# Kernel tuning notes

Hardware: AMD Instinct MI355X
Metric: run time of the kernel (lower is better)

## Reference

```python
import jax, jax.numpy as jnp
import numpy as np

B = 2
D_MODEL = 256
D_FFN = 1024
N_LEVELS = 4
N_HEADS = 8
N_POINTS = 4
D_HEAD = D_MODEL // N_HEADS
SHAPES = np.array([[128, 128], [64, 64], [32, 32], [16, 16]], dtype=np.int32)  # (H, W) per level
LEN = int(SHAPES.prod(axis=1).sum())  # 21760
EPS = 1e-5


def _layer_norm(x, g, b):
    m = jnp.mean(x, axis=-1, keepdims=True)
    v = jnp.mean(jnp.square(x - m), axis=-1, keepdims=True)
    return (x - m) * jax.lax.rsqrt(v + EPS) * g + b


def _bilinear_gather(v_l, loc, H, W):
    # v_l: [B, H*W, NH, DH]; loc: [B, L, NH, NP, 2] in normalized [0,1] coords (x, y)
    # grid_sample(align_corners=False, padding_mode=zeros) semantics: pixel = loc * size - 0.5
    x = loc[..., 0] * W - 0.5
    y = loc[..., 1] * H - 0.5
    x0 = jnp.floor(x)
    y0 = jnp.floor(y)
    dx = x - x0
    dy = y - y0
    x0i = x0.astype(jnp.int32)
    y0i = y0.astype(jnp.int32)
    b_ix = jnp.arange(v_l.shape[0])[:, None, None, None]
    h_ix = jnp.arange(v_l.shape[2])[None, None, :, None]

    def corner(xi, yi, w):
        valid = (xi >= 0) & (xi < W) & (yi >= 0) & (yi < H)
        idx = jnp.clip(yi, 0, H - 1) * W + jnp.clip(xi, 0, W - 1)
        v = v_l[b_ix, idx, h_ix]  # [B, L, NH, NP, DH]
        return v * (w * valid.astype(v.dtype))[..., None]

    return (corner(x0i, y0i, (1 - dx) * (1 - dy))
            + corner(x0i + 1, y0i, dx * (1 - dy))
            + corner(x0i, y0i + 1, (1 - dx) * dy)
            + corner(x0i + 1, y0i + 1, dx * dy))


def _forward(src, pos, reference_points,
             w_off, b_off, w_attn, b_attn, w_val, b_val, w_out, b_out,
             ln1_g, ln1_b, w1, b1, w2, b2, ln2_g, ln2_b,
             spatial_shapes, level_start_index, padding_mask):
    shapes = np.asarray(spatial_shapes)        # static per-level (H, W)
    starts = np.asarray(level_start_index)     # static level offsets
    Bsz, L, _ = src.shape

    # ---- MSDeformAttn ----
    q = src + pos                              # with_pos_embed
    value = src @ w_val + b_val
    value = jnp.where(padding_mask[..., None], 0.0, value)
    value = value.reshape(Bsz, L, N_HEADS, D_HEAD)

    off = (q @ w_off + b_off).reshape(Bsz, L, N_HEADS, N_LEVELS, N_POINTS, 2)
    attn = (q @ w_attn + b_attn).reshape(Bsz, L, N_HEADS, N_LEVELS * N_POINTS)
    attn = jax.nn.softmax(attn, axis=-1).reshape(Bsz, L, N_HEADS, N_LEVELS, N_POINTS)

    wh = jnp.asarray(shapes[:, ::-1].copy(), dtype=src.dtype)  # [NL, 2] = (W, H)
    loc = reference_points[:, :, None, :, None, :] + off / wh[None, None, None, :, None, :]

    out = jnp.zeros((Bsz, L, N_HEADS, D_HEAD), src.dtype)
    for l in range(N_LEVELS):
        H, W = int(shapes[l, 0]), int(shapes[l, 1])
        s = int(starts[l])
        v_l = value[:, s:s + H * W]                          # [B, H*W, NH, DH]
        sampled = _bilinear_gather(v_l, loc[:, :, :, l], H, W)  # [B, L, NH, NP, DH]
        out = out + (sampled * attn[:, :, :, l][..., None]).sum(axis=3)
    attn_out = out.reshape(Bsz, L, D_MODEL) @ w_out + b_out

    # ---- residual + LN + FFN + residual + LN (dropout = identity in eval) ----
    x = _layer_norm(src + attn_out, ln1_g, ln1_b)
    ffn = jax.nn.relu(x @ w1 + b1) @ w2 + b2
    return _layer_norm(x + ffn, ln2_g, ln2_b)


def setup_inputs() -> dict:
    key = jax.random.key(0)
    ks = jax.random.split(key, 16)
    s = 0.02
    n_off = N_HEADS * N_LEVELS * N_POINTS
    level_start = np.concatenate([[0], SHAPES.prod(axis=1).cumsum()[:-1]]).astype(np.int32)
    return {
        "src": jax.random.normal(ks[0], (B, LEN, D_MODEL), jnp.float32),
        "pos": jax.random.normal(ks[1], (B, LEN, D_MODEL), jnp.float32),
        "reference_points": jax.random.uniform(ks[2], (B, LEN, N_LEVELS, 2), jnp.float32),
        "spatial_shapes": jnp.asarray(SHAPES),
        "level_start_index": jnp.asarray(level_start),
        "padding_mask": jnp.zeros((B, LEN), jnp.bool_),
        "w_off": jax.random.normal(ks[3], (D_MODEL, n_off * 2), jnp.float32) * s,
        "b_off": jax.random.normal(ks[4], (n_off * 2,), jnp.float32) * 0.5,
        "w_attn": jax.random.normal(ks[5], (D_MODEL, n_off), jnp.float32) * s,
        "b_attn": jnp.zeros((n_off,), jnp.float32),
        "w_val": jax.random.normal(ks[6], (D_MODEL, D_MODEL), jnp.float32) * s,
        "b_val": jnp.zeros((D_MODEL,), jnp.float32),
        "w_out": jax.random.normal(ks[7], (D_MODEL, D_MODEL), jnp.float32) * s,
        "b_out": jnp.zeros((D_MODEL,), jnp.float32),
        "ln1_g": jnp.ones((D_MODEL,), jnp.float32),
        "ln1_b": jnp.zeros((D_MODEL,), jnp.float32),
        "w1": jax.random.normal(ks[8], (D_MODEL, D_FFN), jnp.float32) * s,
        "b1": jnp.zeros((D_FFN,), jnp.float32),
        "w2": jax.random.normal(ks[9], (D_FFN, D_MODEL), jnp.float32) * s,
        "b2": jnp.zeros((D_MODEL,), jnp.float32),
        "ln2_g": jnp.ones((D_MODEL,), jnp.float32),
        "ln2_b": jnp.zeros((D_MODEL,), jnp.float32),
    }


def reference(src, pos, reference_points, spatial_shapes, level_start_index, padding_mask,
              w_off, b_off, w_attn, b_attn, w_val, b_val, w_out, b_out,
              ln1_g, ln1_b, w1, b1, w2, b2, ln2_g, ln2_b):
    return _forward(src, pos, reference_points,
                    w_off, b_off, w_attn, b_attn, w_val, b_val, w_out, b_out,
                    ln1_g, ln1_b, w1, b1, w2, b2, ln2_g, ln2_b,
                    spatial_shapes, level_start_index, padding_mask)
```

## Files before the change

kernel.cpp:

```cpp
#include <hip/hip_runtime.h>
#include <hip/hip_bf16.h>

#define BSZ      2
#define LTOK     21760
#define NTOK     (BSZ * LTOK)
#define DMODEL   256
#define DFFN     1024

typedef __attribute__((ext_vector_type(8))) short short8;
typedef __attribute__((ext_vector_type(4))) float f32x4;

__device__ __forceinline__ unsigned short f2bf(float x) {
    __hip_bfloat16 h = __float2bfloat16(x);
    return *reinterpret_cast<unsigned short*>(&h);
}
__device__ __forceinline__ float bf2f(unsigned short u) {
    union { unsigned int i; float f; } c; c.i = ((unsigned int)u) << 16; return c.f;
}
__device__ __forceinline__ float bflo(unsigned int u) {
    union { unsigned int i; float f; } c; c.i = u << 16; return c.f;
}
__device__ __forceinline__ float bfhi(unsigned int u) {
    union { unsigned int i; float f; } c; c.i = u & 0xffff0000u; return c.f;
}

__device__ __forceinline__ void gload_lds16(const void* g, void* l) {
    __builtin_amdgcn_global_load_lds(
        (const __attribute__((address_space(1))) unsigned int*)g,
        (__attribute__((address_space(3))) unsigned int*)l, 16, 0, 0);
}

#define TM 128
#define TN 256
#define TBK 32
#define BUFSZ (TM * TBK + TN * TBK)
#define EBS 264

__device__ __forceinline__ void stage_tile(
    const unsigned short* aR0, const unsigned short* aR1,
    const unsigned short* bR0, const unsigned short* bR1,
    const unsigned short* bR2, const unsigned short* bR3,
    int k0, unsigned short* sA, unsigned short* sB, int sr)
{
    gload_lds16(aR0 + k0, &sA[(sr + 0)  * 512]);
    gload_lds16(aR1 + k0, &sA[(sr + 4)  * 512]);
    gload_lds16(bR0 + k0, &sB[(sr + 0)  * 512]);
    gload_lds16(bR1 + k0, &sB[(sr + 4)  * 512]);
    gload_lds16(bR2 + k0, &sB[(sr + 8)  * 512]);
    gload_lds16(bR3 + k0, &sB[(sr + 12) * 512]);
}

__device__ __forceinline__ void compute_tile(
    const unsigned short* sA, const unsigned short* sB,
    int lane, int wm, int wn, f32x4 acc[4][8])
{
    short8 af[4], bfr[8];
    #pragma unroll
    for (int i = 0; i < 4; ++i)
        af[i] = *(const short8*)&sA[(wm * 4 + i) * 512 + lane * 8];
    #pragma unroll
    for (int j = 0; j < 8; ++j)
        bfr[j] = *(const short8*)&sB[(wn * 8 + j) * 512 + lane * 8];
    #pragma unroll
    for (int i = 0; i < 4; ++i)
        #pragma unroll
        for (int j = 0; j < 8; ++j)
            acc[i][j] = __builtin_amdgcn_mfma_f32_16x16x32_bf16(
                af[i], bfr[j], acc[i][j], 0, 0, 0);
}

__device__ __forceinline__ void gemm_core(
    const unsigned short* __restrict__ A,
    const unsigned short* __restrict__ Bt,
    unsigned short* smem,
    int bm, int bn, int N, int K,
    int tid, int lane, int wm, int wn,
    f32x4 acc[4][8])
{
    const int sr = tid >> 6;
    const int fr = lane & 15;
    const int fk = (lane >> 4) * 8;

    const unsigned short* aR0 = A + (size_t)(bm + (sr + 0) * 16 + fr) * K + fk;
    const unsigned short* aR1 = A + (size_t)(bm + (sr + 4) * 16 + fr) * K + fk;
    const unsigned short* bR0 = Bt + (size_t)min(bn + (sr + 0)  * 16 + fr, N - 1) * K + fk;
    const unsigned short* bR1 = Bt + (size_t)min(bn + (sr + 4)  * 16 + fr, N - 1) * K + fk;
    const unsigned short* bR2 = Bt + (size_t)min(bn + (sr + 8)  * 16 + fr, N - 1) * K + fk;
    const unsigned short* bR3 = Bt + (size_t)min(bn + (sr + 12) * 16 + fr, N - 1) * K + fk;

    unsigned short* sA0 = smem;
    unsigned short* sB0 = smem + TM * TBK;
    unsigned short* sA1 = smem + BUFSZ;
    unsigned short* sB1 = smem + BUFSZ + TM * TBK;

    stage_tile(aR0, aR1, bR0, bR1, bR2, bR3, 0, sA0, sB0, sr);
    __syncthreads();

    for (int k0 = 0; k0 < K; k0 += 2 * TBK) {
        if (k0 + TBK < K)
            stage_tile(aR0, aR1, bR0, bR1, bR2, bR3, k0 + TBK, sA1, sB1, sr);
        compute_tile(sA0, sB0, lane, wm, wn, acc);
        __syncthreads();
        if (k0 + 2 * TBK < K)
            stage_tile(aR0, aR1, bR0, bR1, bR2, bR3, k0 + 2 * TBK, sA0, sB0, sr);
        compute_tile(sA1, sB1, lane, wm, wn, acc);
        __syncthreads();
    }
}

__global__ __launch_bounds__(256, 2) void gemm_mfma(
    const unsigned short* __restrict__ A,
    const unsigned short* __restrict__ Bt, const float* __restrict__ bias,
    unsigned short* __restrict__ Cb,
    int M, int N, int K, int relu)
{
    __shared__ __align__(16) unsigned short smem[2 * BUFSZ];
    const int tid  = threadIdx.x;
    const int lane = tid & 63;
    const int wave = tid >> 6;
    const int wm = wave >> 1, wn = wave & 1;
    const int bm = blockIdx.y * TM;
    const int bn = blockIdx.x * TN;

    f32x4 acc[4][8];
    #pragma unroll
    for (int i = 0; i < 4; ++i)
        #pragma unroll
        for (int j = 0; j < 8; ++j)
            acc[i][j] = (f32x4){0.f, 0.f, 0.f, 0.f};

    gemm_core(A, Bt, smem, bm, bn, N, K, tid, lane, wm, wn, acc);

    const int r0 = (lane >> 4) * 4;
    const int c0 = lane & 15;
    unsigned short* eb = smem;
    #pragma unroll
    for (int i = 0; i < 4; ++i) {
        if (i) __syncthreads();
        #pragma unroll
        for (int j = 0; j < 8; ++j) {
            const int col = bn + wn * 128 + j * 16 + c0;
            const float bj = (col < N) ? bias[col] : 0.f;
            #pragma unroll
            for (int r = 0; r < 4; ++r) {
                float v = acc[i][j][r] + bj;
                if (relu) v = fmaxf(v, 0.f);
                eb[(wm * 16 + r0 + r) * EBS + wn * 128 + j * 16 + c0] = f2bf(v);
            }
        }
        __syncthreads();
        #pragma unroll
        for (int qq = 0; qq < 4; ++qq) {
            const int q  = tid + qq * 256;
            const int rl = q >> 5;
            const int ch = q & 31;
            const int grow = bm + (rl >> 4) * 64 + i * 16 + (rl & 15);
            const int colb = bn + ch * 8;
            if (colb < N)
                *(uint4*)&Cb[(size_t)grow * N + colb] =
                    *(const uint4*)&eb[rl * EBS + ch * 8];
        }
    }
}

__global__ __launch_bounds__(256, 2) void gemm_proj(
    const unsigned short* __restrict__ A0, const unsigned short* __restrict__ B0,
    const float* __restrict__ bias0, unsigned short* __restrict__ C0,
    const unsigned char* __restrict__ mask,
    const unsigned short* __restrict__ A1, const unsigned short* __restrict__ B1,
    const float* __restrict__ bias1, unsigned short* __restrict__ C1)
{
    __shared__ __align__(16) unsigned short smem[2 * BUFSZ];
    const int tid  = threadIdx.x;
    const int lane = tid & 63;
    const int wave = tid >> 6;
    const int wm = wave >> 1, wn = wave & 1;
    const int bm = blockIdx.y * TM;
    const int bx = blockIdx.x;

    const int isv = (bx == 0);
    const unsigned short* A    = isv ? A0 : A1;
    const unsigned short* Bt   = isv ? B0 : B1;
    const float*          bias = isv ? bias0 : bias1;
    const int N  = isv ? 256 : 384;
    const int bn = isv ? 0 : (bx - 1) * 256;
    const int K  = 256;

    f32x4 acc[4][8];
    #pragma unroll
    for (int i = 0; i < 4; ++i)
        #pragma unroll
        for (int j = 0; j < 8; ++j)
            acc[i][j] = (f32x4){0.f, 0.f, 0.f, 0.f};

    gemm_core(A, Bt, smem, bm, bn, N, K, tid, lane, wm, wn, acc);

    const int r0 = (lane >> 4) * 4;
    const int c0 = lane & 15;
    unsigned short* eb = smem;
    #pragma unroll
    for (int i = 0; i < 4; ++i) {
        if (i) __syncthreads();
        #pragma unroll
        for (int j = 0; j < 8; ++j) {
            const int col = bn + wn * 128 + j * 16 + c0;
            const float bj = (col < N) ? bias[col] : 0.f;
            #pragma unroll
            for (int r = 0; r < 4; ++r) {
                const int row = bm + wm * 64 + i * 16 + r0 + r;
                float v = acc[i][j][r] + bj;
                if (isv && mask[row]) v = 0.f;
                eb[(wm * 16 + r0 + r) * EBS + wn * 128 + j * 16 + c0] = f2bf(v);
            }
        }
        __syncthreads();
        #pragma unroll
        for (int qq = 0; qq < 4; ++qq) {
            const int q  = tid + qq * 256;
            const int rl = q >> 5;
            const int ch = q & 31;
            const int grow = bm + (rl >> 4) * 64 + i * 16 + (rl & 15);
            const int colb = bn + ch * 8;
            if (colb < N) {
                const uint4 val = *(const uint4*)&eb[rl * EBS + ch * 8];
                if (isv) {
                    const int bb   = grow >= LTOK;
                    const int srow = grow - bb * LTOK;
                    const int hcol = ch >> 2;
                    const int d    = (ch & 3) * 8;
                    *(uint4*)&C0[((size_t)(bb * 8 + hcol) * LTOK + srow) * 32 + d] = val;
                } else {
                    *(uint4*)&C1[(size_t)grow * 384 + colb] = val;
                }
            }
        }
    }
}

__global__ __launch_bounds__(256, 2) void gemm_ln(
    const unsigned short* __restrict__ A,
    const unsigned short* __restrict__ Bt, const float* __restrict__ bias,
    const unsigned short* __restrict__ resid,
    const float* __restrict__ g, const float* __restrict__ be,
    float* __restrict__ outF, unsigned short* __restrict__ outB, int K)
{
    __shared__ __align__(16) unsigned short smem[2 * BUFSZ];
    const int tid  = threadIdx.x;
    const int lane = tid & 63;
    const int wave = tid >> 6;
    const int wm = wave >> 1, wn = wave & 1;
    const int bm = blockIdx.y * TM;

    f32x4 acc[4][8];
    #pragma unroll
    for (int i = 0; i < 4; ++i)
        #pragma unroll
        for (int j = 0; j < 8; ++j)
            acc[i][j] = (f32x4){0.f, 0.f, 0.f, 0.f};

    gemm_core(A, Bt, smem, bm, 0, 256, K, tid, lane, wm, wn, acc);

    const int r0 = (lane >> 4) * 4;
    const int c0 = lane & 15;
    unsigned short* eb = smem;

    #pragma unroll
    for (int i = 0; i < 4; ++i) {
        if (i) __syncthreads();
        #pragma unroll
        for (int j = 0; j < 8; ++j) {
            const int col = wn * 128 + j * 16 + c0;
            const float bj = bias[col];
            #pragma unroll
            for (int r = 0; r < 4; ++r)
                eb[(wm * 16 + r0 + r) * EBS + col] = f2bf(acc[i][j][r] + bj);
        }
        __syncthreads();

        const int row = tid >> 3;
        const int l   = tid & 7;
        const int grow = bm + (row >> 4) * 64 + i * 16 + (row & 15);
        const unsigned short* rr = resid + (size_t)grow * 256 + l * 32;

        float s = 0.f, sq = 0.f;
        #pragma unroll
        for (int k = 0; k < 4; ++k) {
            const uint4 e = *(const uint4*)&eb[row * EBS + l * 32 + k * 8];
            const uint4 rv = *(const uint4*)(rr + k * 8);
            const unsigned int eu[4] = {e.x, e.y, e.z, e.w};
            const unsigned int ru[4] = {rv.x, rv.y, rv.z, rv.w};
            #pragma unroll
            for (int q = 0; q < 4; ++q) {
                const float v0 = bflo(eu[q]) + bflo(ru[q]);
                const float v1 = bfhi(eu[q]) + bfhi(ru[q]);
                s += v0 + v1;
                sq += v0 * v0 + v1 * v1;
            }
        }
        #pragma unroll
        for (int m = 4; m; m >>= 1) {
            s  += __shfl_xor(s, m, 8);
            sq += __shfl_xor(sq, m, 8);
        }
        const float mean = s * (1.f / 256.f);
        const float var  = sq * (1.f / 256.f) - mean * mean;
        const float rs   = rsqrtf(var + 1e-5f);

        #pragma unroll
        for (int k = 0; k < 4; ++k) {
            const int col = l * 32 + k * 8;
            const uint4 e = *(const uint4*)&eb[row * EBS + col];
            const uint4 rv = *(const uint4*)(rr + k * 8);
            const unsigned int eu[4] = {e.x, e.y, e.z, e.w};
            const unsigned int ru[4] = {rv.x, rv.y, rv.z, rv.w};
            float o[8];
            #pragma unroll
            for (int q = 0; q < 4; ++q) {
                const float g0 = g[col + q * 2],     b0 = be[col + q * 2];
                const float g1 = g[col + q * 2 + 1], b1 = be[col + q * 2 + 1];
                o[q * 2]     = (bflo(eu[q]) + bflo(ru[q]) - mean) * rs * g0 + b0;
                o[q * 2 + 1] = (bfhi(eu[q]) + bfhi(ru[q]) - mean) * rs * g1 + b1;
            }
            if (outB) {
                uint4 pk;
                pk.x = (unsigned)f2bf(o[0]) | ((unsigned)f2bf(o[1]) << 16);
                pk.y = (unsigned)f2bf(o[2]) | ((unsigned)f2bf(o[3]) << 16);
                pk.z = (unsigned)f2bf(o[4]) | ((unsigned)f2bf(o[5]) << 16);
                pk.w = (unsigned)f2bf(o[6]) | ((unsigned)f2bf(o[7]) << 16);
                *(uint4*)(outB + (size_t)grow * 256 + col) = pk;
            } else {
                float4 f0 = make_float4(o[0], o[1], o[2], o[3]);
                float4 f1 = make_float4(o[4], o[5], o[6], o[7]);
                *(float4*)(outF + (size_t)grow * 256 + col) = f0;
                *(float4*)(outF + (size_t)grow * 256 + col + 4) = f1;
            }
        }
        __syncthreads();
    }
}

__global__ __launch_bounds__(256) void prepass(
    const float* __restrict__ src, const float* __restrict__ pos,
    unsigned short* __restrict__ sb, unsigned short* __restrict__ qs)
{
    const size_t i = ((size_t)blockIdx.x * 256 + threadIdx.x) * 4;
    const float4 s = *(const float4*)(src + i);
    const float4 p = *(const float4*)(pos + i);
    ushort4 us, uq;
    us.x = f2bf(s.x); us.y = f2bf(s.y); us.z = f2bf(s.z); us.w = f2bf(s.w);
    uq.x = f2bf(s.x + p.x); uq.y = f2bf(s.y + p.y);
    uq.z = f2bf(s.z + p.z); uq.w = f2bf(s.w + p.w);
    *(ushort4*)(sb + i) = us;
    *(ushort4*)(qs + i) = uq;
}

__global__ void transpose_all(
    const float* __restrict__ w_val, const float* __restrict__ w_off,
    const float* __restrict__ w_att, const float* __restrict__ w_out,
    const float* __restrict__ w1,    const float* __restrict__ w2,
    const float* __restrict__ b_off, const float* __restrict__ b_att,
    unsigned short* __restrict__ wvalT, unsigned short* __restrict__ woaT,
    unsigned short* __restrict__ woutT, unsigned short* __restrict__ w1T,
    unsigned short* __restrict__ w2T,   float* __restrict__ bcat)
{
    const int blk = blockIdx.x;
    const int tx = threadIdx.x, ty = threadIdx.y;
    if (blk == 736) {
        const int t = ty * 32 + tx;
        bcat[t] = (t < 256) ? b_off[t] : b_att[t - 256];
        if (t + 256 < 384) bcat[t + 256] = b_att[t];
        return;
    }
    const float* W; unsigned short* Wt; int K, N, base;
    if      (blk < 64)  { W = w_val; Wt = wvalT;           K = 256;  N = 256;  base = 0;   }
    else if (blk < 128) { W = w_off; Wt = woaT;            K = 256;  N = 256;  base = 64;  }
    else if (blk < 160) { W = w_att; Wt = woaT + 256*256;  K = 256;  N = 128;  base = 128; }
    else if (blk < 224) { W = w_out; Wt = woutT;           K = 256;  N = 256;  base = 160; }
    else if (blk < 480) { W = w1;    Wt = w1T;             K = 256;  N = 1024; base = 224; }
    else                { W = w2;    Wt = w2T;             K = 1024; N = 256;  base = 480; }
    const int local = blk - base;
    const int kb = local % (K / 32);
    const int nb = local / (K / 32);
    const int k0 = kb * 32, n0 = nb * 32;

    __shared__ float t[32][33];
    #pragma unroll
    for (int i = 0; i < 32; i += 8)
        t[ty + i][tx] = W[(size_t)(k0 + ty + i) * N + n0 + tx];
    __syncthreads();
    #pragma unroll
    for (int i = 0; i < 32; i += 8)
        Wt[(size_t)(n0 + ty + i) * K + k0 + tx] = f2bf(t[tx][ty + i]);
}

__global__ __launch_bounds__(256) void sample_kernel(
    const unsigned short* __restrict__ vT, const unsigned short* __restrict__ qp,
    const float* __restrict__ ref,
    const int* __restrict__ sshapes, const int* __restrict__ lstart,
    unsigned short* __restrict__ samp)
{
    __shared__ __align__(16) int   s_o[256][4];
    __shared__ __align__(16) float s_w[256][4];

    const int blk   = blockIdx.x;
    const int plane = blk & 15;
    const int chunk = blk >> 4;
    const int b = plane >> 3;
    const int h = plane & 7;
    const int s0 = chunk * 16;
    const int t = threadIdx.x;

    {
        const int tl = t >> 4;
        const int p  = t & 15;
        const int l  = p >> 2;
        const int pp = p & 3;
        const int H = sshapes[2 * l], W = sshapes[2 * l + 1];
        const float Wf = (float)W, Hf = (float)H;
        const size_t tok = (size_t)(b * LTOK + s0 + tl);

        const float ox = bf2f(qp[tok * 384 + h * 32 + l * 8 + pp * 2 + 0]);
        const float oy = bf2f(qp[tok * 384 + h * 32 + l * 8 + pp * 2 + 1]);
        const float rx = ref[tok * 8 + l * 2 + 0];
        const float ry = ref[tok * 8 + l * 2 + 1];

        const float x = (rx + ox / Wf) * Wf - 0.5f;
        const float y = (ry + oy / Hf) * Hf - 0.5f;
        const float x0 = floorf(x), y0 = floorf(y);
        const float dx = x - x0, dy = y - y0;
        const int x0i = (int)x0, y0i = (int)y0;
        const int s = lstart[l];

        const float a = bf2f(qp[tok * 384 + 256 + h * 16 + p]);
        float mx = a;
        #pragma unroll
        for (int m = 8; m; m >>= 1) mx = fmaxf(mx, __shfl_xor(mx, m, 16));
        const float e = __expf(a - mx);
        float ssum = e;
        #pragma unroll
        for (int m = 8; m; m >>= 1) ssum += __shfl_xor(ssum, m, 16);
        const float prob = e / ssum;

        const float cw[4] = {(1.f - dx) * (1.f - dy), dx * (1.f - dy),
                             (1.f - dx) * dy,         dx * dy};
        const int cx[4] = {x0i, x0i + 1, x0i,     x0i + 1};
        const int cy[4] = {y0i, y0i,     y0i + 1, y0i + 1};
        int4   o4;
        float4 w4;
        #pragma unroll
        for (int c = 0; c < 4; ++c) {
            const bool valid = (cx[c] >= 0) & (cx[c] < W) & (cy[c] >= 0) & (cy[c] < H);
            const int xi = min(max(cx[c], 0), W - 1);
            const int yi = min(max(cy[c], 0), H - 1);
            ((int*)&o4)[c]   = (s + yi * W + xi) * 64;
            ((float*)&w4)[c] = valid ? cw[c] * prob : 0.f;
        }
        const int r = p * 16 + tl;
        *(int4*)&s_o[r][0]   = o4;
        *(float4*)&s_w[r][0] = w4;
    }
    __syncthreads();

    const int tl = t >> 4;
    const int dp = t & 15;
    const char* vp = (const char*)(vT + (size_t)plane * LTOK * 32) + dp * 4;
    float acc0 = 0.f, acc1 = 0.f;
    #pragma unroll
    for (int p = 0; p < 16; ++p) {
        const int r = p * 16 + tl;
        const int4   o4 = *(const int4*)&s_o[r][0];
        const float4 w4 = *(const float4*)&s_w[r][0];
        const unsigned int u0 = *(const unsigned int*)(vp + o4.x);
        const unsigned int u1 = *(const unsigned int*)(vp + o4.y);
        const unsigned int u2 = *(const unsigned int*)(vp + o4.z);
        const unsigned int u3 = *(const unsigned int*)(vp + o4.w);
        acc0 = fmaf(w4.x, bflo(u0), acc0); acc1 = fmaf(w4.x, bfhi(u0), acc1);
        acc0 = fmaf(w4.y, bflo(u1), acc0); acc1 = fmaf(w4.y, bfhi(u1), acc1);
        acc0 = fmaf(w4.z, bflo(u2), acc0); acc1 = fmaf(w4.z, bfhi(u2), acc1);
        acc0 = fmaf(w4.w, bflo(u3), acc0); acc1 = fmaf(w4.w, bfhi(u3), acc1);
    }
    const unsigned int o = (unsigned)f2bf(acc0) | ((unsigned)f2bf(acc1) << 16);
    *(unsigned int*)(samp + (size_t)(b * LTOK + s0 + tl) * 256 + h * 32 + dp * 2) = o;
}

extern "C" void kernel_launch(void* const* d_in, const int* in_sizes, int n_in,
                              void* d_out, int out_size, void* d_ws, size_t ws_size,
                              hipStream_t stream)
{
    const float* src   = (const float*)d_in[0];
    const float* pos   = (const float*)d_in[1];
    const float* ref   = (const float*)d_in[2];
    const int*   sshap = (const int*)d_in[3];
    const int*   lstrt = (const int*)d_in[4];
    const unsigned char* mask = (const unsigned char*)d_in[5];
    const float* w_off = (const float*)d_in[6];
    const float* b_off = (const float*)d_in[7];
    const float* w_att = (const float*)d_in[8];
    const float* b_att = (const float*)d_in[9];
    const float* w_val = (const float*)d_in[10];
    const float* b_val = (const float*)d_in[11];
    const float* w_out = (const float*)d_in[12];
    const float* b_out = (const float*)d_in[13];
    const float* ln1g  = (const float*)d_in[14];
    const float* ln1b  = (const float*)d_in[15];
    const float* w1    = (const float*)d_in[16];
    const float* b1    = (const float*)d_in[17];
    const float* w2    = (const float*)d_in[18];
    const float* b2    = (const float*)d_in[19];
    const float* ln2g  = (const float*)d_in[20];
    const float* ln2b  = (const float*)d_in[21];
    float* out = (float*)d_out;

    const size_t HSZ = (size_t)NTOK * 256 * 2;
    char* w = (char*)d_ws;
    unsigned short* qs     = (unsigned short*)w;
    unsigned short* samp16 = (unsigned short*)w;
    unsigned short* qpb    = (unsigned short*)(w + HSZ);
    unsigned short* vT     = (unsigned short*)(w + HSZ * 5 / 2);
    unsigned short* hidb   = (unsigned short*)w;
    unsigned short* sb     = (unsigned short*)(w + HSZ * 9 / 2);
    unsigned short* xb     = (unsigned short*)(w + HSZ * 11 / 2);
    char* wreg = w + HSZ * 13 / 2;
    unsigned short* wvalT  = (unsigned short*)wreg;
    unsigned short* woaT   = wvalT + 256 * 256;
    unsigned short* woutT  = woaT + 384 * 256;
    unsigned short* w1T    = woutT + 256 * 256;
    unsigned short* w2T    = w1T + 1024 * 256;
    float*          bcat   = (float*)(w2T + 256 * 1024);

    const dim3 blk(256);

    prepass<<<dim3(NTOK / 4), blk, 0, stream>>>(src, pos, sb, qs);

    transpose_all<<<dim3(737), dim3(32, 8), 0, stream>>>(
        w_val, w_off, w_att, w_out, w1, w2, b_off, b_att,
        wvalT, woaT, woutT, w1T, w2T, bcat);

    gemm_proj<<<dim3(3, NTOK / TM), blk, 0, stream>>>(
        sb, wvalT, b_val, vT, mask, qs, woaT, bcat, qpb);

    sample_kernel<<<dim3(16 * (LTOK / 16)), blk, 0, stream>>>(
        vT, qpb, ref, sshap, lstrt, samp16);

    gemm_ln<<<dim3(1, NTOK / TM), blk, 0, stream>>>(
        samp16, woutT, b_out, sb, ln1g, ln1b, nullptr, xb, 256);

    gemm_mfma<<<dim3(4, NTOK / TM), blk, 0, stream>>>(
        xb, w1T, b1, hidb, NTOK, DFFN, 256, 1);

    gemm_ln<<<dim3(1, NTOK / TM), blk, 0, stream>>>(
        hidb, w2T, b2, xb, ln2g, ln2b, out, nullptr, DFFN);
}
```

Before: 482.6 us.

## Fuse FFN up-projection, ReLU, down-projection and LayerNorm into one kernel

Replaces the separate W1 GEMM (writing a bf16 hidden tensor to global memory) and the W2 GEMM+LayerNorm kernel with a single kernel. Each block keeps a 64-row input tile in LDS, computes 128-column hidden chunks with ReLU into LDS, and accumulates them into the W2 output in registers, then applies residual add and LayerNorm. This removes the global write and re-read of the 1024-wide hidden activation and one launch. In exchange it uses a smaller M tile (64 rows), a larger LDS footprint, and many block-wide barriers, with weights re-streamed per block.

```diff
diff --git a/kernel.cpp b/kernel.cpp
--- a/kernel.cpp
+++ b/kernel.cpp
@@ -105,61 +105,6 @@
             stage_tile(aR0, aR1, bR0, bR1, bR2, bR3, k0 + 2 * TBK, sA0, sB0, sr);
         compute_tile(sA1, sB1, lane, wm, wn, acc);
         __syncthreads();
-    }
-}
-
-__global__ __launch_bounds__(256, 2) void gemm_mfma(
-    const unsigned short* __restrict__ A,
-    const unsigned short* __restrict__ Bt, const float* __restrict__ bias,
-    unsigned short* __restrict__ Cb,
-    int M, int N, int K, int relu)
-{
-    __shared__ __align__(16) unsigned short smem[2 * BUFSZ];
-    const int tid  = threadIdx.x;
-    const int lane = tid & 63;
-    const int wave = tid >> 6;
-    const int wm = wave >> 1, wn = wave & 1;
-    const int bm = blockIdx.y * TM;
-    const int bn = blockIdx.x * TN;
-
-    f32x4 acc[4][8];
-    #pragma unroll
-    for (int i = 0; i < 4; ++i)
-        #pragma unroll
-        for (int j = 0; j < 8; ++j)
-            acc[i][j] = (f32x4){0.f, 0.f, 0.f, 0.f};
-
-    gemm_core(A, Bt, smem, bm, bn, N, K, tid, lane, wm, wn, acc);
-
-    const int r0 = (lane >> 4) * 4;
-    const int c0 = lane & 15;
-    unsigned short* eb = smem;
-    #pragma unroll
-    for (int i = 0; i < 4; ++i) {
-        if (i) __syncthreads();
-        #pragma unroll
-        for (int j = 0; j < 8; ++j) {
-            const int col = bn + wn * 128 + j * 16 + c0;
-            const float bj = (col < N) ? bias[col] : 0.f;
-            #pragma unroll
-            for (int r = 0; r < 4; ++r) {
-                float v = acc[i][j][r] + bj;
-                if (relu) v = fmaxf(v, 0.f);
-                eb[(wm * 16 + r0 + r) * EBS + wn * 128 + j * 16 + c0] = f2bf(v);
-            }
-        }
-        __syncthreads();
-        #pragma unroll
-        for (int qq = 0; qq < 4; ++qq) {
-            const int q  = tid + qq * 256;
-            const int rl = q >> 5;
-            const int ch = q & 31;
-            const int grow = bm + (rl >> 4) * 64 + i * 16 + (rl & 15);
-            const int colb = bn + ch * 8;
-            if (colb < N)
-                *(uint4*)&Cb[(size_t)grow * N + colb] =
-                    *(const uint4*)&eb[rl * EBS + ch * 8];
-        }
     }
 }
 
@@ -334,6 +279,215 @@
                 *(float4*)(outF + (size_t)grow * 256 + col) = f0;
                 *(float4*)(outF + (size_t)grow * 256 + col + 4) = f1;
             }
+        }
+        __syncthreads();
+    }
+}
+
+#define FTM 64
+
+__device__ __forceinline__ void ffn_f1(
+    const unsigned short* sxb, const unsigned short* buf, int ks,
+    int lane, int wm, int wn, f32x4 acc1[2][4])
+{
+    short8 af[2], bfr[4];
+    #pragma unroll
+    for (int i = 0; i < 2; ++i)
+        af[i] = *(const short8*)&sxb[ks * 2048 + (wm * 2 + i) * 512 + lane * 8];
+    #pragma unroll
+    for (int j = 0; j < 4; ++j)
+        bfr[j] = *(const short8*)&buf[(wn * 4 + j) * 512 + lane * 8];
+    #pragma unroll
+    for (int i = 0; i < 2; ++i)
+        #pragma unroll
+        for (int j = 0; j < 4; ++j)
+            acc1[i][j] = __builtin_amdgcn_mfma_f32_16x16x32_bf16(
+                af[i], bfr[j], acc1[i][j], 0, 0, 0);
+}
+
+__device__ __forceinline__ void ffn_f2(
+    const unsigned short* hidA, const unsigned short* buf, int ks,
+    int lane, int wm, int wn, f32x4 acc2[2][8])
+{
+    short8 af[2], bfr[8];
+    #pragma unroll
+    for (int i = 0; i < 2; ++i)
+        af[i] = *(const short8*)&hidA[ks * 2048 + (wm * 2 + i) * 512 + lane * 8];
+    #pragma unroll
+    for (int j = 0; j < 8; ++j)
+        bfr[j] = *(const short8*)&buf[(wn * 8 + j) * 512 + lane * 8];
+    #pragma unroll
+    for (int i = 0; i < 2; ++i)
+        #pragma unroll
+        for (int j = 0; j < 8; ++j)
+            acc2[i][j] = __builtin_amdgcn_mfma_f32_16x16x32_bf16(
+                af[i], bfr[j], acc2[i][j], 0, 0, 0);
+}
+
+__global__ __launch_bounds__(256, 2) void ffn_fused(
+    const unsigned short* __restrict__ xb,
+    const unsigned short* __restrict__ w1T,
+    const float* __restrict__ b1,
+    const unsigned short* __restrict__ w2T,
+    const float* __restrict__ b2,
+    const float* __restrict__ g, const float* __restrict__ be,
+    float* __restrict__ outF)
+{
+    __shared__ __align__(16) unsigned short smem[40960];
+    unsigned short* sxb  = smem;
+    unsigned short* hidA = smem + 16384;
+    unsigned short* bs0  = smem + 24576;
+    unsigned short* bs1  = smem + 32768;
+
+    const int tid  = threadIdx.x;
+    const int lane = tid & 63;
+    const int wave = tid >> 6;
+    const int wm = wave >> 1, wn = wave & 1;
+    const int bm = blockIdx.x * FTM;
+    const int fr = lane & 15;
+    const int fk = (lane >> 4) * 8;
+    const int sr = wave;
+
+    const unsigned short* xrow = xb + (size_t)(bm + sr * 16 + fr) * 256 + fk;
+    const unsigned short* w1b0 = w1T + (size_t)((sr + 0) * 16 + fr) * 256 + fk;
+    const unsigned short* w1b1 = w1T + (size_t)((sr + 4) * 16 + fr) * 256 + fk;
+    const unsigned short* w2b0 = w2T + (size_t)((sr + 0)  * 16 + fr) * 1024 + fk;
+    const unsigned short* w2b1 = w2T + (size_t)((sr + 4)  * 16 + fr) * 1024 + fk;
+    const unsigned short* w2b2 = w2T + (size_t)((sr + 8)  * 16 + fr) * 1024 + fk;
+    const unsigned short* w2b3 = w2T + (size_t)((sr + 12) * 16 + fr) * 1024 + fk;
+
+    f32x4 acc2[2][8];
+    #pragma unroll
+    for (int i = 0; i < 2; ++i)
+        #pragma unroll
+        for (int j = 0; j < 8; ++j)
+            acc2[i][j] = (f32x4){0.f, 0.f, 0.f, 0.f};
+
+    const int r0 = (lane >> 4) * 4;
+    const int c0 = lane & 15;
+
+    #pragma unroll
+    for (int kc = 0; kc < 8; ++kc)
+        gload_lds16(xrow + kc * 32, &sxb[kc * 2048 + sr * 512]);
+    gload_lds16(w1b0, &bs0[(sr + 0) * 512]);
+    gload_lds16(w1b1, &bs0[(sr + 4) * 512]);
+    __syncthreads();
+
+    #define STG_B1(c_, ks_, buf_)                                            \
+        gload_lds16(w1b0 + (c_) * 32768 + (ks_) * 32, &buf_[(sr + 0) * 512]);\
+        gload_lds16(w1b1 + (c_) * 32768 + (ks_) * 32, &buf_[(sr + 4) * 512]);
+    #define STG_B2(c_, ks_, buf_)                                            \
+        gload_lds16(w2b0 + (c_) * 128 + (ks_) * 32, &buf_[(sr + 0)  * 512]); \
+        gload_lds16(w2b1 + (c_) * 128 + (ks_) * 32, &buf_[(sr + 4)  * 512]); \
+        gload_lds16(w2b2 + (c_) * 128 + (ks_) * 32, &buf_[(sr + 8)  * 512]); \
+        gload_lds16(w2b3 + (c_) * 128 + (ks_) * 32, &buf_[(sr + 12) * 512]);
+
+    for (int c = 0; c < 8; ++c) {
+        f32x4 acc1[2][4];
+        #pragma unroll
+        for (int i = 0; i < 2; ++i)
+            #pragma unroll
+            for (int j = 0; j < 4; ++j)
+                acc1[i][j] = (f32x4){0.f, 0.f, 0.f, 0.f};
+
+        STG_B1(c, 1, bs1); ffn_f1(sxb, bs0, 0, lane, wm, wn, acc1); __syncthreads();
+        STG_B1(c, 2, bs0); ffn_f1(sxb, bs1, 1, lane, wm, wn, acc1); __syncthreads();
+        STG_B1(c, 3, bs1); ffn_f1(sxb, bs0, 2, lane, wm, wn, acc1); __syncthreads();
+        STG_B1(c, 4, bs0); ffn_f1(sxb, bs1, 3, lane, wm, wn, acc1); __syncthreads();
+        STG_B1(c, 5, bs1); ffn_f1(sxb, bs0, 4, lane, wm, wn, acc1); __syncthreads();
+        STG_B1(c, 6, bs0); ffn_f1(sxb, bs1, 5, lane, wm, wn, acc1); __syncthreads();
+        STG_B1(c, 7, bs1); ffn_f1(sxb, bs0, 6, lane, wm, wn, acc1); __syncthreads();
+        STG_B2(c, 0, bs0); ffn_f1(sxb, bs1, 7, lane, wm, wn, acc1); __syncthreads();
+
+        #pragma unroll
+        for (int j = 0; j < 4; ++j) {
+            const int colj = wn * 64 + j * 16 + c0;
+            const float bj = b1[c * 128 + colj];
+            const int kc2  = colj >> 5;
+            const int sel  = (colj >> 3) & 3;
+            const int c7   = colj & 7;
+            #pragma unroll
+            for (int i = 0; i < 2; ++i) {
+                const int base = kc2 * 2048 + (wm * 2 + i) * 512
+                               + (r0 | (sel << 4)) * 8 + c7;
+                #pragma unroll
+                for (int r = 0; r < 4; ++r)
+                    hidA[base + r * 8] = f2bf(fmaxf(acc1[i][j][r] + bj, 0.f));
+            }
+        }
+        __syncthreads();
+
+        STG_B2(c, 1, bs1); ffn_f2(hidA, bs0, 0, lane, wm, wn, acc2); __syncthreads();
+        STG_B2(c, 2, bs0); ffn_f2(hidA, bs1, 1, lane, wm, wn, acc2); __syncthreads();
+        STG_B2(c, 3, bs1); ffn_f2(hidA, bs0, 2, lane, wm, wn, acc2); __syncthreads();
+        if (c < 7) { STG_B1(c + 1, 0, bs0); }
+        ffn_f2(hidA, bs1, 3, lane, wm, wn, acc2); __syncthreads();
+    }
+    #undef STG_B1
+    #undef STG_B2
+
+    unsigned short* eb = smem;
+    #pragma unroll
+    for (int i = 0; i < 2; ++i) {
+        if (i) __syncthreads();
+        #pragma unroll
+        for (int j = 0; j < 8; ++j) {
+            const int col = wn * 128 + j * 16 + c0;
+            const float bj = b2[col];
+            #pragma unroll
+            for (int r = 0; r < 4; ++r)
+                eb[(wm * 16 + r0 + r) * EBS + col] = f2bf(acc2[i][j][r] + bj);
+        }
+        __syncthreads();
+
+        const int row = tid >> 3;
+        const int l   = tid & 7;
+        const int grow = bm + (row >> 4) * 32 + i * 16 + (row & 15);
+        const unsigned short* rr = xb + (size_t)grow * 256 + l * 32;
+
+        float s = 0.f, sq = 0.f;
+        #pragma unroll
+        for (int k = 0; k < 4; ++k) {
+            const uint4 e = *(const uint4*)&eb[row * EBS + l * 32 + k * 8];
+            const uint4 rv = *(const uint4*)(rr + k * 8);
+            const unsigned int eu[4] = {e.x, e.y, e.z, e.w};
+            const unsigned int ru[4] = {rv.x, rv.y, rv.z, rv.w};
+            #pragma unroll
+            for (int q = 0; q < 4; ++q) {
+                const float v0 = bflo(eu[q]) + bflo(ru[q]);
+                const float v1 = bfhi(eu[q]) + bfhi(ru[q]);
+                s += v0 + v1;
+                sq += v0 * v0 + v1 * v1;
+            }
+        }
+        #pragma unroll
+        for (int m = 4; m; m >>= 1) {
+            s  += __shfl_xor(s, m, 8);
+            sq += __shfl_xor(sq, m, 8);
+        }
+        const float mean = s * (1.f / 256.f);
+        const float var  = sq * (1.f / 256.f) - mean * mean;
+        const float rs   = rsqrtf(var + 1e-5f);
+
+        #pragma unroll
+        for (int k = 0; k < 4; ++k) {
+            const int col = l * 32 + k * 8;
+            const uint4 e = *(const uint4*)&eb[row * EBS + col];
+            const uint4 rv = *(const uint4*)(rr + k * 8);
+            const unsigned int eu[4] = {e.x, e.y, e.z, e.w};
+            const unsigned int ru[4] = {rv.x, rv.y, rv.z, rv.w};
+            float o[8];
+            #pragma unroll
+            for (int q = 0; q < 4; ++q) {
+                const float g0 = g[col + q * 2],     b0 = be[col + q * 2];
+                const float g1 = g[col + q * 2 + 1], b1v = be[col + q * 2 + 1];
+                o[q * 2]     = (bflo(eu[q]) + bflo(ru[q]) - mean) * rs * g0 + b0;
+                o[q * 2 + 1] = (bfhi(eu[q]) + bfhi(ru[q]) - mean) * rs * g1 + b1v;
+            }
+            float4 f0 = make_float4(o[0], o[1], o[2], o[3]);
+            float4 f1 = make_float4(o[4], o[5], o[6], o[7]);
+            *(float4*)(outF + (size_t)grow * 256 + col) = f0;
+            *(float4*)(outF + (size_t)grow * 256 + col + 4) = f1;
         }
         __syncthreads();
     }
@@ -517,7 +671,6 @@
     unsigned short* samp16 = (unsigned short*)w;
     unsigned short* qpb    = (unsigned short*)(w + HSZ);
     unsigned short* vT     = (unsigned short*)(w + HSZ * 5 / 2);
-    unsigned short* hidb   = (unsigned short*)w;
     unsigned short* sb     = (unsigned short*)(w + HSZ * 9 / 2);
     unsigned short* xb     = (unsigned short*)(w + HSZ * 11 / 2);
     char* wreg = w + HSZ * 13 / 2;
@@ -545,9 +698,6 @@
     gemm_ln<<<dim3(1, NTOK / TM), blk, 0, stream>>>(
         samp16, woutT, b_out, sb, ln1g, ln1b, nullptr, xb, 256);
 
-    gemm_mfma<<<dim3(4, NTOK / TM), blk, 0, stream>>>(
-        xb, w1T, b1, hidb, NTOK, DFFN, 256, 1);
-
-    gemm_ln<<<dim3(1, NTOK / TM), blk, 0, stream>>>(
-        hidb, w2T, b2, xb, ln2g, ln2b, out, nullptr, DFFN);
-}
+    ffn_fused<<<dim3(NTOK / FTM), blk, 0, stream>>>(
+        xb, w1T, b1, w2T, b2, ln2g, ln2b, out);
+}
```

After: 492.6 us. 1.02x slower.
